# Performance work log

Measured on AMD Instinct MI355X. Metric: run time of the kernel, lower is better.

## Reference

```python
import jax, jax.numpy as jnp
import numpy as np

B, VOCAB, F = 4096, 50000, 64


def setup_inputs() -> dict:
    key = jax.random.key(0)
    k1, k2 = jax.random.split(key, 2)
    # binary multi-hot input (row > 0 mask semantics of the original)
    x = jax.random.randint(k1, (B, VOCAB), 0, 2, dtype=jnp.int32)
    # truncated-normal-ish init for the factor embedding table
    V = (jax.random.normal(k2, (VOCAB, F), dtype=jnp.float32) * 0.05)
    # linear (first-order) bias table is zero-initialized in the original
    bias = jnp.zeros((VOCAB, 1), dtype=jnp.float32)
    g_bias = jnp.zeros((), dtype=jnp.float32)
    return {"x": x, "V": V, "bias": bias, "g_bias": g_bias}


def reference(x, V, bias, g_bias):
    # x: [B, VOCAB] binary multi-hot; V: [VOCAB, F]; bias: [VOCAB, 1]; g_bias: scalar
    xf = x.astype(V.dtype)
    # FM sum-square identity: for selected rows S = {i : x_i > 0},
    # 0.5 * (sum_{i,j in S} <v_i, v_j> - sum_{i in S} ||v_i||^2)
    #   = 0.5 * (||sum_i v_i||^2 - sum_i ||v_i||^2)
    xv = xf @ V                                   # [B, F] = sum of selected rows
    sum_sq = jnp.sum(xv * xv, axis=-1)            # [B]
    sq_sum = xf @ jnp.sum(V * V, axis=-1)         # [B]
    second_order = 0.5 * (sum_sq - sq_sum)        # [B]
    linear = g_bias + xf @ bias                   # [B, 1]
    return linear + second_order[:, None]         # [B, 1]
```

## Files before the change

### kernel.cpp

```cpp
#include <hip/hip_runtime.h>

#define VOCAB 50000
#define BROWS 4096
#define F 64
#define NCOLS 80
#define NT 5
#define SPLITS 16
#define NR 98
#define KT_TOTAL (SPLITS * NR)
#define KPAD (KT_TOTAL * 32)
#define RDWORDS 1568
#define SPANS 25

#define AS1 __attribute__((address_space(1)))
#define AS3 __attribute__((address_space(3)))

typedef __attribute__((ext_vector_type(4))) float f32x4;
typedef __attribute__((ext_vector_type(8))) short s16x8;

__device__ __forceinline__ unsigned short f2bf(float f) {
    unsigned u = __builtin_bit_cast(unsigned, f);
    unsigned r = (u + 0x7FFFu + ((u >> 16) & 1u)) >> 16;
    return (unsigned short)r;
}
__device__ __forceinline__ float bf2f(unsigned short b) {
    unsigned u = ((unsigned)b) << 16;
    return __builtin_bit_cast(float, u);
}

__global__ void fm_pack(const int* __restrict__ x, unsigned* __restrict__ xb) {
    const int W = blockIdx.x * 4 + (threadIdx.x >> 6);
    const int lane = threadIdx.x & 63;
    const int row = W / SPANS;
    const int span = W - row * SPANS;
    const int* __restrict__ xr = x + (size_t)row * VOCAB + span * 2048;
    unsigned my = 0;
    if (span < SPANS - 1) {
#pragma unroll
        for (int j = 0; j < 32; ++j) {
            int v = xr[j * 64 + lane];
            unsigned long long m = __ballot(v & 1);
            if ((lane >> 1) == j) my = (lane & 1) ? (unsigned)(m >> 32) : (unsigned)m;
        }
        xb[(size_t)row * RDWORDS + span * 64 + lane] = my;
    } else {
        const int base = (SPANS - 1) * 2048;
#pragma unroll
        for (int j = 0; j < 14; ++j) {
            int idx = base + j * 64 + lane;
            int v = (idx < VOCAB) ? xr[j * 64 + lane] : 0;
            unsigned long long m = __ballot(v & 1);
            if ((lane >> 1) == j) my = (lane & 1) ? (unsigned)(m >> 32) : (unsigned)m;
        }
        const int d = (SPANS - 1) * 64 + lane;
        if (d < RDWORDS) xb[(size_t)row * RDWORDS + d] = my;
    }
}

__global__ void fm_prep_w(const float* __restrict__ V, const float* __restrict__ bias,
                          float* __restrict__ w) {
    int k = blockIdx.x * blockDim.x + threadIdx.x;
    if (k >= KPAD) return;
    float val = 0.f;
    if (k < VOCAB) {
        const float4* row = reinterpret_cast<const float4*>(V + (size_t)k * F);
        float ss = 0.f;
#pragma unroll
        for (int j = 0; j < F / 4; ++j) {
            float4 v = row[j];
            ss += v.x * v.x + v.y * v.y + v.z * v.z + v.w * v.w;
        }
        val = bias[k] - 0.5f * ss;
    }
    w[k] = val;
}

__global__ void fm_prep_bfrag(const float* __restrict__ V, const float* __restrict__ w,
                              uint4* __restrict__ bfrag) {
    int t = blockIdx.x * blockDim.x + threadIdx.x;
    if (t >= KT_TOTAL * NT * 64) return;
    int lane = t & 63;
    int tile = t >> 6;
    int nt = tile % NT;
    int kt = tile / NT;
    int n = nt * 16 + (lane & 15);
    int kbase = kt * 32 + (lane >> 4) * 8;
    unsigned short o[8];
#pragma unroll
    for (int j = 0; j < 8; ++j) {
        int k = kbase + j;
        float v = 0.f;
        if (k < VOCAB) {
            if (n < F) {
                v = V[(size_t)k * F + n];
            } else if (n == F) {
                v = w[k];
            } else if (n == F + 1) {
                float wv = w[k];
                v = wv - bf2f(f2bf(wv));
            }
        }
        o[j] = f2bf(v);
    }
    uint4 pk;
    pk.x = (unsigned)o[0] | ((unsigned)o[1] << 16);
    pk.y = (unsigned)o[2] | ((unsigned)o[3] << 16);
    pk.z = (unsigned)o[4] | ((unsigned)o[5] << 16);
    pk.w = (unsigned)o[6] | ((unsigned)o[7] << 16);
    bfrag[t] = pk;
}

__global__ __launch_bounds__(256, 4) void fm_main(const unsigned* __restrict__ xb,
                                                  const uint4* __restrict__ bfrag,
                                                  float* __restrict__ part) {
    __shared__ uint4 bbuf[2][NT * 64];
    const int bx = blockIdx.x;
    const int split = bx & (SPLITS - 1);
    const int mblock = bx >> 4;
    const int tid = threadIdx.x;
    const int wave = tid >> 6;
    const int lane = tid & 63;
    const int kb = lane >> 4;
    const int rowA = mblock * 64 + wave * 16 + (lane & 15);
    const int kt0 = split * NR;
    const unsigned* __restrict__ xp = xb + (size_t)rowA * RDWORDS + kt0;
    const int e0 = (wave << 6) + lane;

    auto stage = [&](int rnd) {
        const uint4* src = bfrag + (size_t)(kt0 + rnd) * (NT * 64);
        uint4* dst = bbuf[rnd & 1];
        __builtin_amdgcn_global_load_lds((const AS1 void*)(src + e0),
                                         (AS3 void*)(dst + (wave << 6)), 16, 0, 0);
        if (wave == 0)
            __builtin_amdgcn_global_load_lds((const AS1 void*)(src + 256 + lane),
                                             (AS3 void*)(dst + 256), 16, 0, 0);
    };
    auto unpack = [&](unsigned m) -> s16x8 {
        uint4 apk;
        apk.x = ((m & 1u)   ? 0x3F80u : 0u) | ((m & 2u)   ? 0x3F800000u : 0u);
        apk.y = ((m & 4u)   ? 0x3F80u : 0u) | ((m & 8u)   ? 0x3F800000u : 0u);
        apk.z = ((m & 16u)  ? 0x3F80u : 0u) | ((m & 32u)  ? 0x3F800000u : 0u);
        apk.w = ((m & 64u)  ? 0x3F80u : 0u) | ((m & 128u) ? 0x3F800000u : 0u);
        return __builtin_bit_cast(s16x8, apk);
    };

    f32x4 acc[NT];
#pragma unroll
    for (int nt = 0; nt < NT; ++nt) acc[nt] = (f32x4){0.f, 0.f, 0.f, 0.f};

    stage(0);
    unsigned cd = xp[0];
    __syncthreads();

    for (int r = 0; r < NR; ++r) {
        unsigned nd = 0;
        if (r + 1 < NR) {
            stage(r + 1);
            nd = xp[r + 1];
        }
        s16x8 af = unpack((cd >> (kb * 8)) & 0xFFu);
        const uint4* bb = bbuf[r & 1];
#pragma unroll
        for (int nt = 0; nt < NT; ++nt) {
            s16x8 bf = __builtin_bit_cast(s16x8, bb[nt * 64 + lane]);
            acc[nt] = __builtin_amdgcn_mfma_f32_16x16x32_bf16(af, bf, acc[nt], 0, 0, 0);
        }
        __syncthreads();
        cd = nd;
    }

    float* __restrict__ p = part + (size_t)split * BROWS * NCOLS;
    int m0 = mblock * 64 + wave * 16 + kb * 4;
    int c0 = lane & 15;
#pragma unroll
    for (int nt = 0; nt < NT; ++nt)
#pragma unroll
        for (int r = 0; r < 4; ++r)
            p[(size_t)(m0 + r) * NCOLS + nt * 16 + c0] = acc[nt][r];
}

__global__ void fm_reduce(const float* __restrict__ part, const float* __restrict__ gbias,
                          float* __restrict__ out) {
    int b = blockIdx.x * 4 + (threadIdx.x >> 6);
    int lane = threadIdx.x & 63;
    float acc = 0.f;
#pragma unroll
    for (int s = 0; s < SPLITS; ++s)
        acc += part[((size_t)s * BROWS + b) * NCOLS + lane];
    float sq = acc * acc;
    float ex = 0.f;
    if (lane < 16)       ex = part[((size_t)lane * BROWS + b) * NCOLS + F];
    else if (lane < 32)  ex = part[((size_t)(lane - 16) * BROWS + b) * NCOLS + F + 1];
#pragma unroll
    for (int off = 32; off; off >>= 1) {
        sq += __shfl_xor(sq, off, 64);
        ex += __shfl_xor(ex, off, 64);
    }
    if (lane == 0) out[b] = gbias[0] + ex + 0.5f * sq;
}

extern "C" void kernel_launch(void* const* d_in, const int* in_sizes, int n_in,
                              void* d_out, int out_size, void* d_ws, size_t ws_size,
                              hipStream_t stream) {
    const int*   x     = (const int*)d_in[0];
    const float* V     = (const float*)d_in[1];
    const float* bias  = (const float*)d_in[2];
    const float* gbias = (const float*)d_in[3];
    float* out = (float*)d_out;

    char* ws = (char*)d_ws;
    unsigned* xbw = (unsigned*)ws;
    uint4* bfrag  = (uint4*)(ws + (size_t)BROWS * RDWORDS * 4);
    float* w      = (float*)(ws + (size_t)BROWS * RDWORDS * 4 + (size_t)KT_TOTAL * NT * 64 * 16);
    float* part   = (float*)(ws + (size_t)BROWS * RDWORDS * 4 + (size_t)KT_TOTAL * NT * 64 * 16
                             + (size_t)KPAD * 4);

    fm_pack<<<(BROWS * SPANS) / 4, 256, 0, stream>>>(x, xbw);
    fm_prep_w<<<(KPAD + 255) / 256, 256, 0, stream>>>(V, bias, w);
    fm_prep_bfrag<<<(KT_TOTAL * NT * 64 + 255) / 256, 256, 0, stream>>>(V, w, bfrag);
    fm_main<<<(BROWS / 64) * SPLITS, 256, 0, stream>>>(xbw, bfrag, part);
    fm_reduce<<<BROWS / 4, 256, 0, stream>>>(part, gbias, out);
}
```

Measured before the change: 236.8 us.

## Vectorize bit-packing with int4 loads and permute B-fragment vocab order to match

The pack kernel now reads four ints per lane with 16-byte vector loads and builds each mask word from nibbles, replacing 32 ballot rounds per span. This changes which vocab indices each bit represents, so the B-fragment prep kernel remaps each packed position back to its real vocab index. RDWORDS and NR are padded to a full 25 spans, so the main loop runs slightly more k-tiles. The aim is to cut the cost of the bandwidth-heavy pass over the 800MB int input.

```diff
diff --git a/kernel.cpp b/kernel.cpp
--- a/kernel.cpp
+++ b/kernel.cpp
@@ -6,10 +6,10 @@
 #define NCOLS 80
 #define NT 5
 #define SPLITS 16
-#define NR 98
+#define NR 100
 #define KT_TOTAL (SPLITS * NR)
 #define KPAD (KT_TOTAL * 32)
-#define RDWORDS 1568
+#define RDWORDS 1600
 #define SPANS 25
 
 #define AS1 __attribute__((address_space(1)))
@@ -27,34 +27,41 @@
     unsigned u = ((unsigned)b) << 16;
     return __builtin_bit_cast(float, u);
 }
+
 
 __global__ void fm_pack(const int* __restrict__ x, unsigned* __restrict__ xb) {
     const int W = blockIdx.x * 4 + (threadIdx.x >> 6);
     const int lane = threadIdx.x & 63;
     const int row = W / SPANS;
     const int span = W - row * SPANS;
-    const int* __restrict__ xr = x + (size_t)row * VOCAB + span * 2048;
+    const int ebase = span * 2048;
+    const int* __restrict__ xr = x + (size_t)row * VOCAB + ebase;
     unsigned my = 0;
     if (span < SPANS - 1) {
 #pragma unroll
-        for (int j = 0; j < 32; ++j) {
-            int v = xr[j * 64 + lane];
-            unsigned long long m = __ballot(v & 1);
-            if ((lane >> 1) == j) my = (lane & 1) ? (unsigned)(m >> 32) : (unsigned)m;
-        }
-        xb[(size_t)row * RDWORDS + span * 64 + lane] = my;
+        for (int j = 0; j < 8; ++j) {
+            int4 v = *reinterpret_cast<const int4*>(xr + j * 256 + lane * 4);
+            unsigned nib = (unsigned)(v.x & 1) | ((unsigned)(v.y & 1) << 1)
+                         | ((unsigned)(v.z & 1) << 2) | ((unsigned)(v.w & 1) << 3);
+            my |= nib << (4 * j);
+        }
     } else {
-        const int base = (SPANS - 1) * 2048;
-#pragma unroll
-        for (int j = 0; j < 14; ++j) {
-            int idx = base + j * 64 + lane;
-            int v = (idx < VOCAB) ? xr[j * 64 + lane] : 0;
-            unsigned long long m = __ballot(v & 1);
-            if ((lane >> 1) == j) my = (lane & 1) ? (unsigned)(m >> 32) : (unsigned)m;
-        }
-        const int d = (SPANS - 1) * 64 + lane;
-        if (d < RDWORDS) xb[(size_t)row * RDWORDS + d] = my;
-    }
+#pragma unroll
+        for (int j = 0; j < 8; ++j) {
+            const int e0 = ebase + j * 256 + lane * 4;
+            unsigned nib = 0;
+            if (e0 + 4 <= VOCAB) {
+                int4 v = *reinterpret_cast<const int4*>(xr + j * 256 + lane * 4);
+                nib = (unsigned)(v.x & 1) | ((unsigned)(v.y & 1) << 1)
+                    | ((unsigned)(v.z & 1) << 2) | ((unsigned)(v.w & 1) << 3);
+            } else if (e0 < VOCAB) {
+                for (int c = 0; c < VOCAB - e0; ++c)
+                    nib |= (unsigned)(xr[j * 256 + lane * 4 + c] & 1) << c;
+            }
+            my |= nib << (4 * j);
+        }
+    }
+    xb[(size_t)row * RDWORDS + span * 64 + lane] = my;
 }
 
 __global__ void fm_prep_w(const float* __restrict__ V, const float* __restrict__ bias,
@@ -84,19 +91,22 @@
     int nt = tile % NT;
     int kt = tile / NT;
     int n = nt * 16 + (lane & 15);
-    int kbase = kt * 32 + (lane >> 4) * 8;
+    int kvbase = kt * 32 + (lane >> 4) * 8;
     unsigned short o[8];
 #pragma unroll
     for (int j = 0; j < 8; ++j) {
-        int k = kbase + j;
+        int kv = kvbase + j;
+        int span = kv >> 11, loc = kv & 2047;
+        int l = loc >> 5, p = loc & 31;
+        int e = (span << 11) | ((p >> 2) << 8) | (l << 2) | (p & 3);
         float v = 0.f;
-        if (k < VOCAB) {
+        if (e < VOCAB) {
             if (n < F) {
-                v = V[(size_t)k * F + n];
+                v = V[(size_t)e * F + n];
             } else if (n == F) {
-                v = w[k];
+                v = w[e];
             } else if (n == F + 1) {
-                float wv = w[k];
+                float wv = w[e];
                 v = wv - bf2f(f2bf(wv));
             }
         }
```

After: 238.7 us. No clear change (+0.8%).
